# Kernel tuning notes

Hardware: AMD Instinct MI355X
Metric: run time of the kernel (lower is better)

Reference implementation:

```python
import jax, jax.numpy as jnp
import numpy as np

V, E, H = 32000, 128, 256
B, L, T = 32, 512, 64


def _lstm_scan(x_pre, Whh, h0, c0):
    # x_pre: [L, B, 4H] precomputed input projection (+bias). PyTorch gate order i,f,g,o.
    def step(carry, xp):
        h, c = carry
        g = xp + h @ Whh.T
        i, f, gg, o = jnp.split(g, 4, axis=-1)
        c = jax.nn.sigmoid(f) * c + jax.nn.sigmoid(i) * jnp.tanh(gg)
        h = jax.nn.sigmoid(o) * jnp.tanh(c)
        return (h, c), h
    (h, c), hs = jax.lax.scan(step, (h0, c0), x_pre)
    return hs, h, c


def setup_inputs() -> dict:
    key = jax.random.key(0)
    ks = jax.random.split(key, 20)
    s = 0.05  # ~ uniform(-1/sqrt(H), 1/sqrt(H)) scale
    def rn(k, shape):
        return (jax.random.normal(k, shape) * s).astype(jnp.float32)
    return {
        "source": jax.random.randint(ks[0], (B, L), 0, V),
        "target": jax.random.randint(ks[1], (B, T), 0, V),
        "embedding": rn(ks[2], (V, E)),
        "enc_fw_Wih": rn(ks[3], (4 * H, E)),
        "enc_fw_Whh": rn(ks[4], (4 * H, H)),
        "enc_fw_b": rn(ks[5], (4 * H,)),
        "enc_bw_Wih": rn(ks[6], (4 * H, E)),
        "enc_bw_Whh": rn(ks[7], (4 * H, H)),
        "enc_bw_b": rn(ks[8], (4 * H,)),
        "dec_Wih": rn(ks[9], (4 * H, E + 2 * H)),
        "dec_Whh": rn(ks[10], (4 * H, H)),
        "dec_b": rn(ks[11], (4 * H,)),
        "attn_w": rn(ks[12], (4 * H,)),
        "attn_b": rn(ks[13], (1,)),
        "dp_W": rn(ks[14], (2 * H, H)),
        "dp_b": rn(ks[15], (2 * H,)),
        "vp_W": rn(ks[16], (V, 3 * H)),
        "vp_b": rn(ks[17], (V,)),
        "pg_W": rn(ks[18], (3 * H + E, 1)),
        "pg_b": rn(ks[19], (1,)),
    }


def _forward(source, target, embedding, enc_fw_Wih, enc_fw_Whh, enc_fw_b,
             enc_bw_Wih, enc_bw_Whh, enc_bw_b, dec_Wih, dec_Whh, dec_b,
             attn_w, attn_b, dp_W, dp_b, vp_W, vp_b, pg_W, pg_b):
    Bn = source.shape[0]
    emb = embedding[source]                                   # [B,L,E]
    h0 = jnp.zeros((Bn, H), jnp.float32)
    c0 = jnp.zeros((Bn, H), jnp.float32)
    # bidirectional encoder
    xpf = jnp.swapaxes(emb @ enc_fw_Wih.T + enc_fw_b, 0, 1)   # [L,B,4H]
    hs_f, h_f, c_f = _lstm_scan(xpf, enc_fw_Whh, h0, c0)
    xpb = jnp.swapaxes(emb @ enc_bw_Wih.T + enc_bw_b, 0, 1)[::-1]
    hs_b, _, _ = _lstm_scan(xpb, enc_bw_Whh, h0, c0)
    enc_out = jnp.concatenate([hs_f, hs_b[::-1]], axis=-1)    # [L,B,2H]
    enc_out = jnp.swapaxes(enc_out, 0, 1)                     # [B,L,2H]

    # attn Linear(4H->1) split into encoder part (precomputed) and decoder part
    wa_enc, wa_dec = attn_w[:2 * H], attn_w[2 * H:]
    enc_att = enc_out @ wa_enc                                # [B,L]
    batch_idx = jnp.arange(Bn)[:, None]

    # teacher forcing: input at step t is target[:, t-1], zeros at t=0
    tokens_in = jnp.concatenate(
        [jnp.zeros((Bn, 1), target.dtype), target[:, :-1]], axis=1).T  # [T,B]

    def step(carry, tok):
        h, c = carry
        emb_t = embedding[tok]                                # [B,E]
        dec_proj = h @ dp_W.T + dp_b                          # [B,2H]
        score = enc_att + (dec_proj @ wa_dec)[:, None] + attn_b  # [B,L]
        aw = jax.nn.softmax(score, axis=1)
        context = jnp.einsum('bl,bld->bd', aw, enc_out)       # [B,2H]
        dec_in = jnp.concatenate([emb_t, context], axis=1)    # [B,E+2H]
        g = dec_in @ dec_Wih.T + dec_b + h @ dec_Whh.T
        i, f, gg, o = jnp.split(g, 4, axis=-1)
        c = jax.nn.sigmoid(f) * c + jax.nn.sigmoid(i) * jnp.tanh(gg)
        h = jax.nn.sigmoid(o) * jnp.tanh(c)
        gen_feat = jnp.concatenate([h, context], axis=1)      # [B,3H]
        vocab_dist = jax.nn.softmax(gen_feat @ vp_W.T + vp_b, axis=1)  # [B,V]
        p_gen = jax.nn.sigmoid(
            jnp.concatenate([gen_feat, emb_t], axis=1) @ pg_W + pg_b)  # [B,1]
        copy = jnp.zeros_like(vocab_dist).at[batch_idx, source].add(aw)
        final = p_gen * vocab_dist + (1.0 - p_gen) * copy
        return (h, c), final

    # decoder init = forward-direction final encoder state (matches torch slice)
    _, outs = jax.lax.scan(step, (h_f, c_f), tokens_in)       # [T,B,V]
    return jnp.swapaxes(outs, 0, 1)                           # [B,T,V]


def reference(source, target, embedding, enc_fw_Wih, enc_fw_Whh, enc_fw_b,
              enc_bw_Wih, enc_bw_Whh, enc_bw_b, dec_Wih, dec_Whh, dec_b,
              attn_w, attn_b, dp_W, dp_b, vp_W, vp_b, pg_W, pg_b):
    return _forward(source, target, embedding, enc_fw_Wih, enc_fw_Whh, enc_fw_b,
                    enc_bw_Wih, enc_bw_Whh, enc_bw_b, dec_Wih, dec_Whh, dec_b,
                    attn_w, attn_b, dp_W, dp_b, vp_W, vp_b, pg_W, pg_b)
```

## Files before the change

kernel.cpp:

```cpp
#include <hip/hip_runtime.h>
#include <hip/hip_bf16.h>


#define DEVINL __device__ __forceinline__

typedef _Float16 f16;
typedef _Float16 f16x2 __attribute__((ext_vector_type(2)));
typedef _Float16 f16x8 __attribute__((ext_vector_type(8)));
typedef short    s16x8 __attribute__((ext_vector_type(8)));
typedef float    f32x4 __attribute__((ext_vector_type(4)));
typedef unsigned int u32x4 __attribute__((ext_vector_type(4)));

DEVINL float dot2f(unsigned int a, unsigned int b, float acc) {
#if __has_builtin(__builtin_amdgcn_fdot2)
  return __builtin_amdgcn_fdot2(__builtin_bit_cast(f16x2, a),
                                __builtin_bit_cast(f16x2, b), acc, false);
#else
  f16x2 x = __builtin_bit_cast(f16x2, a);
  f16x2 y = __builtin_bit_cast(f16x2, b);
  return acc + (float)x[0] * (float)y[0] + (float)x[1] * (float)y[1];
#endif
}

DEVINL float sigm(float x) { return 1.0f / (1.0f + __expf(-x)); }
DEVINL float tanh_f(float x) {
  float e = __expf(2.0f * x);
  return (e - 1.0f) / (e + 1.0f);
}
DEVINL unsigned int pack2(float a, float b) {
  f16x2 p; p[0] = (f16)a; p[1] = (f16)b;
  return __builtin_bit_cast(unsigned int, p);
}


__global__ __launch_bounds__(256) void k_pack_whh(const float* __restrict__ W,
                                                  uint4* __restrict__ dst) {
  int id = blockIdx.x * 256 + threadIdx.x;
  int k2b = id >> 10, j = id & 1023;
  const float* s = W + (size_t)j * 256 + k2b * 8;
  uint4 u;
  u.x = pack2(s[0], s[1]); u.y = pack2(s[2], s[3]);
  u.z = pack2(s[4], s[5]); u.w = pack2(s[6], s[7]);
  dst[k2b * 1024 + j] = u;
}

__global__ __launch_bounds__(256) void k_pack_wih(const float* __restrict__ W,
                                                  unsigned int* __restrict__ dst,
                                                  int ldk) {
  int id = blockIdx.x * 256 + threadIdx.x;
  int j = id >> 6, k2 = id & 63;
  dst[j * 64 + k2] = pack2(W[(size_t)j * ldk + 2 * k2],
                           W[(size_t)j * ldk + 2 * k2 + 1]);
}

__global__ __launch_bounds__(256) void k_pack_vpw(const float* __restrict__ W,
                                                  __hip_bfloat16* __restrict__ dst) {
  size_t id = (size_t)blockIdx.x * 256 + threadIdx.x;
  dst[id] = __float2bfloat16(W[id]);
}

__global__ __launch_bounds__(256) void k_encproj(
    const int* __restrict__ source, const float* __restrict__ emb,
    const unsigned int* __restrict__ W2, const float* __restrict__ bias,
    f16* __restrict__ X, int rev) {
  int l = blockIdx.x;
  int tid = threadIdx.x;
  __shared__ int toks[32];
  __shared__ unsigned int e2[32 * 66];
  if (tid < 32) toks[tid] = source[tid * 512 + l];
  __syncthreads();
  {
    int row = tid >> 3;
    int k2b = (tid & 7) * 8;
    const float* er = emb + (size_t)toks[row] * 128 + k2b * 2;
#pragma unroll
    for (int i = 0; i < 8; ++i)
      e2[row * 66 + k2b + i] = pack2(er[2 * i], er[2 * i + 1]);
  }
  __syncthreads();
  int jg = tid >> 3;
  int bq = (tid & 7) * 4;
  int orow = rev ? (511 - l) : l;
  for (int jt = 0; jt < 4; ++jt) {
    int j0 = jt * 256 + jg * 8;
    float acc[8][4];
#pragma unroll
    for (int jj = 0; jj < 8; ++jj) {
      float bv = bias[j0 + jj];
#pragma unroll
      for (int bb = 0; bb < 4; ++bb) acc[jj][bb] = bv;
    }
    for (int kp = 0; kp < 32; ++kp) {
      uint2 w[8], e[4];
#pragma unroll
      for (int jj = 0; jj < 8; ++jj)
        w[jj] = *(const uint2*)(W2 + (size_t)(j0 + jj) * 64 + kp * 2);
#pragma unroll
      for (int bb = 0; bb < 4; ++bb)
        e[bb] = *(const uint2*)(e2 + (bq + bb) * 66 + kp * 2);
#pragma unroll
      for (int jj = 0; jj < 8; ++jj)
#pragma unroll
        for (int bb = 0; bb < 4; ++bb) {
          acc[jj][bb] = dot2f(e[bb].x, w[jj].x, acc[jj][bb]);
          acc[jj][bb] = dot2f(e[bb].y, w[jj].y, acc[jj][bb]);
        }
    }
#pragma unroll
    for (int bb = 0; bb < 4; ++bb) {
      f16x8 v;
#pragma unroll
      for (int jj = 0; jj < 8; ++jj) v[jj] = (f16)acc[jj][bb];
      *(f16x8*)(X + ((size_t)orow * 32 + bq + bb) * 1024 + j0) = v;
    }
  }
}

__global__ __launch_bounds__(256) void k_decproj(
    const int* __restrict__ target, const float* __restrict__ emb,
    const unsigned int* __restrict__ W2, const float* __restrict__ cprj,
    const float* __restrict__ pgW, f16* __restrict__ X,
    float* __restrict__ pemb) {
  int t = blockIdx.x;
  int tid = threadIdx.x;
  __shared__ int toks[32];
  __shared__ unsigned int e2[32 * 66];
  if (tid < 32) toks[tid] = (t == 0) ? 0 : target[tid * 64 + t - 1];
  __syncthreads();
  {
    int row = tid >> 3;
    int k2b = (tid & 7) * 8;
    const float* er = emb + (size_t)toks[row] * 128 + k2b * 2;
#pragma unroll
    for (int i = 0; i < 8; ++i)
      e2[row * 66 + k2b + i] = pack2(er[2 * i], er[2 * i + 1]);
  }
  __syncthreads();
  if (tid < 32) {
    float s = 0.f;
    for (int k2 = 0; k2 < 64; ++k2) {
      f16x2 p = __builtin_bit_cast(f16x2, e2[tid * 66 + k2]);
      s += (float)p[0] * pgW[768 + 2 * k2] + (float)p[1] * pgW[768 + 2 * k2 + 1];
    }
    pemb[t * 32 + tid] = s;
  }
  int jg = tid >> 3;
  int bq = (tid & 7) * 4;
  for (int jt = 0; jt < 4; ++jt) {
    int j0 = jt * 256 + jg * 8;
    float acc[8][4];
#pragma unroll
    for (int jj = 0; jj < 8; ++jj)
#pragma unroll
      for (int bb = 0; bb < 4; ++bb)
        acc[jj][bb] = cprj[(size_t)(bq + bb) * 1024 + j0 + jj];
    for (int kp = 0; kp < 32; ++kp) {
      uint2 w[8], e[4];
#pragma unroll
      for (int jj = 0; jj < 8; ++jj)
        w[jj] = *(const uint2*)(W2 + (size_t)(j0 + jj) * 64 + kp * 2);
#pragma unroll
      for (int bb = 0; bb < 4; ++bb)
        e[bb] = *(const uint2*)(e2 + (bq + bb) * 66 + kp * 2);
#pragma unroll
      for (int jj = 0; jj < 8; ++jj)
#pragma unroll
        for (int bb = 0; bb < 4; ++bb) {
          acc[jj][bb] = dot2f(e[bb].x, w[jj].x, acc[jj][bb]);
          acc[jj][bb] = dot2f(e[bb].y, w[jj].y, acc[jj][bb]);
        }
    }
#pragma unroll
    for (int bb = 0; bb < 4; ++bb) {
      f16x8 v;
#pragma unroll
      for (int jj = 0; jj < 8; ++jj) v[jj] = (f16)acc[jj][bb];
      *(f16x8*)(X + ((size_t)t * 32 + bq + bb) * 1024 + j0) = v;
    }
  }
}

#define PIN23(A)                                                             \
  asm volatile("" : "+v"(A[0]), "+v"(A[1]), "+v"(A[2]), "+v"(A[3]),          \
                    "+v"(A[4]), "+v"(A[5]), "+v"(A[6]), "+v"(A[7]),          \
                    "+v"(A[8]), "+v"(A[9]), "+v"(A[10]), "+v"(A[11]),        \
                    "+v"(A[12]), "+v"(A[13]), "+v"(A[14]), "+v"(A[15]),      \
                    "+v"(A[16]), "+v"(A[17]), "+v"(A[18]), "+v"(A[19]),      \
                    "+v"(A[20]), "+v"(A[21]), "+v"(A[22]))

__global__ __launch_bounds__(256, 1) void k_scan(
    const uint4* __restrict__ Wp0, const f16* __restrict__ X0,
    float* __restrict__ out, float* __restrict__ cf,
    const float* __restrict__ hinit, int mode, int nsteps) {
  extern __shared__ char smem[];
  uint4* WL = (uint4*)smem;
  f16*   hh = (f16*)(smem + 147456);
  int bid = blockIdx.x;
  int dir = (mode == 2) ? 0 : (bid >> 5);
  int b   = (mode == 2) ? bid : (bid & 31);
  int isdec = (mode == 2);
  const uint4* Wp = Wp0 + (size_t)dir * 32768;
  const f16* X = X0 + (size_t)dir * 16777216;
  int t_ = threadIdx.x;

  u32x4 w0[23], w1[23], w2[23], w3[23];
#pragma unroll
  for (int q = 0; q < 23; ++q) {
    w0[q] = *(const u32x4*)&Wp[(q << 10) + 0 * 256 + t_];
    w1[q] = *(const u32x4*)&Wp[(q << 10) + 1 * 256 + t_];
    w2[q] = *(const u32x4*)&Wp[(q << 10) + 2 * 256 + t_];
    w3[q] = *(const u32x4*)&Wp[(q << 10) + 3 * 256 + t_];
  }
  PIN23(w0); PIN23(w1); PIN23(w2); PIN23(w3);

  for (int i = t_; i < 9 * 1024; i += 256) WL[i] = Wp[23 * 1024 + i];

  float c_reg;
  if (isdec) {
    c_reg = cf[b * 256 + t_];
    hh[t_] = (f16)hinit[((size_t)b * 512 + 511) * 512 + t_];
  } else {
    c_reg = 0.f;
    hh[t_] = (f16)0.f;
  }
  __syncthreads();

  const f16* xp = X + (size_t)b * 1024;
  f16 xc0 = xp[t_], xc1 = xp[256 + t_], xc2 = xp[512 + t_], xc3 = xp[768 + t_];

  for (int t = 0; t < nsteps; ++t) {
    float a0 = (float)xc0, a1 = (float)xc1, a2 = (float)xc2, a3 = (float)xc3;
    if (t + 1 < nsteps) {
      const f16* xn = xp + 32768;
      xc0 = xn[t_]; xc1 = xn[256 + t_]; xc2 = xn[512 + t_]; xc3 = xn[768 + t_];
      xp = xn;
    }
    const f16* hb = hh + (t & 1) * 256;
#pragma unroll
    for (int q = 0; q < 23; ++q) {
      u32x4 hq = *(const u32x4*)(hb + q * 8);
      a0 = dot2f(hq[0], w0[q][0], a0); a1 = dot2f(hq[0], w1[q][0], a1);
      a2 = dot2f(hq[0], w2[q][0], a2); a3 = dot2f(hq[0], w3[q][0], a3);
      a0 = dot2f(hq[1], w0[q][1], a0); a1 = dot2f(hq[1], w1[q][1], a1);
      a2 = dot2f(hq[1], w2[q][1], a2); a3 = dot2f(hq[1], w3[q][1], a3);
      a0 = dot2f(hq[2], w0[q][2], a0); a1 = dot2f(hq[2], w1[q][2], a1);
      a2 = dot2f(hq[2], w2[q][2], a2); a3 = dot2f(hq[2], w3[q][2], a3);
      a0 = dot2f(hq[3], w0[q][3], a0); a1 = dot2f(hq[3], w1[q][3], a1);
      a2 = dot2f(hq[3], w2[q][3], a2); a3 = dot2f(hq[3], w3[q][3], a3);
    }
#pragma unroll
    for (int q = 23; q < 32; ++q) {
      u32x4 hq = *(const u32x4*)(hb + q * 8);
      u32x4 v0 = *(const u32x4*)&WL[(q - 23) * 1024 + 0 * 256 + t_];
      u32x4 v1 = *(const u32x4*)&WL[(q - 23) * 1024 + 1 * 256 + t_];
      u32x4 v2 = *(const u32x4*)&WL[(q - 23) * 1024 + 2 * 256 + t_];
      u32x4 v3 = *(const u32x4*)&WL[(q - 23) * 1024 + 3 * 256 + t_];
      a0 = dot2f(hq[0], v0[0], a0); a1 = dot2f(hq[0], v1[0], a1);
      a2 = dot2f(hq[0], v2[0], a2); a3 = dot2f(hq[0], v3[0], a3);
      a0 = dot2f(hq[1], v0[1], a0); a1 = dot2f(hq[1], v1[1], a1);
      a2 = dot2f(hq[1], v2[1], a2); a3 = dot2f(hq[1], v3[1], a3);
      a0 = dot2f(hq[2], v0[2], a0); a1 = dot2f(hq[2], v1[2], a1);
      a2 = dot2f(hq[2], v2[2], a2); a3 = dot2f(hq[2], v3[2], a3);
      a0 = dot2f(hq[3], v0[3], a0); a1 = dot2f(hq[3], v1[3], a1);
      a2 = dot2f(hq[3], v2[3], a2); a3 = dot2f(hq[3], v3[3], a3);
    }
    c_reg = sigm(a1) * c_reg + sigm(a0) * tanh_f(a2);
    float hv = sigm(a3) * tanh_f(c_reg);
    hh[((t + 1) & 1) * 256 + t_] = (f16)hv;
    if (isdec)
      out[((size_t)t * 32 + b) * 256 + t_] = hv;
    else if (dir == 1)
      out[((size_t)b * 512 + (511 - t)) * 512 + 256 + t_] = hv;
    else
      out[((size_t)b * 512 + t) * 512 + t_] = hv;
    __syncthreads();
  }
  if (!isdec && dir == 0) cf[b * 256 + t_] = c_reg;
}

__global__ __launch_bounds__(512) void k_attention(
    const float* __restrict__ enc_out, const float* __restrict__ attn_w,
    const float* __restrict__ pgW, const int* __restrict__ source,
    float* __restrict__ aw_out, float* __restrict__ ctx_out,
    float* __restrict__ pctx, float* __restrict__ copyb) {
  int b = blockIdx.x, tid = threadIdx.x;
  __shared__ float red[512];
  __shared__ float awl[512];
  const float4* row = (const float4*)(enc_out + ((size_t)b * 512 + tid) * 512);
  const float4* wv = (const float4*)attn_w;
  float s = 0.f;
  for (int i = 0; i < 128; ++i) {
    float4 r = row[i], w = wv[i];
    s += r.x * w.x + r.y * w.y + r.z * w.z + r.w * w.w;
  }
  red[tid] = s; __syncthreads();
  for (int off = 256; off > 0; off >>= 1) {
    if (tid < off) red[tid] = fmaxf(red[tid], red[tid + off]);
    __syncthreads();
  }
  float m = red[0]; __syncthreads();
  float e = __expf(s - m);
  red[tid] = e; __syncthreads();
  for (int off = 256; off > 0; off >>= 1) {
    if (tid < off) red[tid] += red[tid + off];
    __syncthreads();
  }
  float a = e / red[0];
  __syncthreads();
  awl[tid] = a;
  aw_out[b * 512 + tid] = a;
  atomicAdd(&copyb[(size_t)b * 32000 + source[b * 512 + tid]], a);
  __syncthreads();
  float c = 0.f;
  const float* col = enc_out + (size_t)b * 512 * 512 + tid;
  for (int ll = 0; ll < 512; ++ll) c += awl[ll] * col[(size_t)ll * 512];
  ctx_out[b * 512 + tid] = c;
  red[tid] = c * pgW[256 + tid];
  __syncthreads();
  for (int off = 256; off > 0; off >>= 1) {
    if (tid < off) red[tid] += red[tid + off];
    __syncthreads();
  }
  if (tid == 0) pctx[b] = red[0];
}

__global__ __launch_bounds__(256) void k_ctxproj(
    const float* __restrict__ ctx, const float* __restrict__ dWih,
    const float* __restrict__ db, float* __restrict__ cprj) {
  int b = blockIdx.x, tid = threadIdx.x;
  __shared__ float cs[512];
  cs[tid] = ctx[b * 512 + tid];
  cs[tid + 256] = ctx[b * 512 + 256 + tid];
  __syncthreads();
  const float4* c4 = (const float4*)cs;
  for (int q = 0; q < 4; ++q) {
    int j = q * 256 + tid;
    const float4* wr = (const float4*)(dWih + (size_t)j * 640 + 128);
    float s = db[j];
    for (int i = 0; i < 128; ++i) {
      float4 w = wr[i]; float4 c = c4[i];
      s += w.x * c.x + w.y * c.y + w.z * c.z + w.w * c.w;
    }
    cprj[b * 1024 + j] = s;
  }
}

__global__ __launch_bounds__(256) void k_pgen_gf(
    const float* __restrict__ h_all, const float* __restrict__ ctx,
    const float* __restrict__ pgW, const float* __restrict__ pgb,
    const float* __restrict__ pctx, const float* __restrict__ pemb,
    float* __restrict__ pgen, __hip_bfloat16* __restrict__ gf) {
  int r = blockIdx.x, tid = threadIdx.x;
  int b = r & 31;
  float h = h_all[(size_t)r * 256 + tid];
  gf[(size_t)r * 768 + tid] = __float2bfloat16(h);
  float c0 = ctx[b * 512 + tid], c1 = ctx[b * 512 + 256 + tid];
  gf[(size_t)r * 768 + 256 + tid] = __float2bfloat16(c0);
  gf[(size_t)r * 768 + 512 + tid] = __float2bfloat16(c1);
  __shared__ float red[256];
  red[tid] = h * pgW[tid];
  __syncthreads();
  for (int off = 128; off > 0; off >>= 1) {
    if (tid < off) red[tid] += red[tid + off];
    __syncthreads();
  }
  if (tid == 0) pgen[r] = sigm(red[0] + pctx[b] + pemb[r] + pgb[0]);
}

__global__ __launch_bounds__(256) void k_logits(
    const __hip_bfloat16* __restrict__ A, const __hip_bfloat16* __restrict__ B,
    const float* __restrict__ vpb, float* __restrict__ out) {
  __shared__ short As[128 * 40];
  __shared__ short Bs[128 * 40];
  int tid = threadIdx.x;
  int bn = blockIdx.x, bm = blockIdx.y;
  int wave = tid >> 6, lane = tid & 63;
  int q = lane >> 4, m = lane & 15;
  f32x4 acc[2][8];
#pragma unroll
  for (int i = 0; i < 2; ++i)
#pragma unroll
    for (int j = 0; j < 8; ++j)
      acc[i][j] = (f32x4){0.f, 0.f, 0.f, 0.f};
  const short* Ag = (const short*)A + (size_t)(bm * 128) * 768;
  const short* Bg = (const short*)B + (size_t)(bn * 128) * 768;
  int lrow = tid >> 2;
  int lseg = (tid & 3) * 8;
  for (int kc = 0; kc < 768; kc += 32) {
    __syncthreads();
    *(s16x8*)&As[lrow * 40 + lseg] = *(const s16x8*)(Ag + (size_t)lrow * 768 + kc + lseg);
    *(s16x8*)&As[(lrow + 64) * 40 + lseg] = *(const s16x8*)(Ag + (size_t)(lrow + 64) * 768 + kc + lseg);
    *(s16x8*)&Bs[lrow * 40 + lseg] = *(const s16x8*)(Bg + (size_t)lrow * 768 + kc + lseg);
    *(s16x8*)&Bs[(lrow + 64) * 40 + lseg] = *(const s16x8*)(Bg + (size_t)(lrow + 64) * 768 + kc + lseg);
    __syncthreads();
    s16x8 a0 = *(const s16x8*)&As[(wave * 32 + m) * 40 + q * 8];
    s16x8 a1 = *(const s16x8*)&As[(wave * 32 + 16 + m) * 40 + q * 8];
#pragma unroll
    for (int nb = 0; nb < 8; ++nb) {
      s16x8 bf = *(const s16x8*)&Bs[(nb * 16 + m) * 40 + q * 8];
      acc[0][nb] = __builtin_amdgcn_mfma_f32_16x16x32_bf16(a0, bf, acc[0][nb], 0, 0, 0);
      acc[1][nb] = __builtin_amdgcn_mfma_f32_16x16x32_bf16(a1, bf, acc[1][nb], 0, 0, 0);
    }
  }
#pragma unroll
  for (int mb = 0; mb < 2; ++mb)
#pragma unroll
    for (int nb = 0; nb < 8; ++nb) {
      int v = bn * 128 + nb * 16 + m;
      float vb = vpb[v];
#pragma unroll
      for (int rg = 0; rg < 4; ++rg) {
        int R = bm * 128 + wave * 32 + mb * 16 + q * 4 + rg;
        int bb = R & 31, tt = R >> 5;
        out[((size_t)bb * 64 + tt) * 32000 + v] = acc[mb][nb][rg] + vb;
      }
    }
}

__global__ __launch_bounds__(256) void k_rowsum(const float* __restrict__ out,
                                                float* __restrict__ invs) {
  int row = blockIdx.x, tid = threadIdx.x;
  const float* r = out + (size_t)row * 32000;
  float s = 0.f;
  for (int i = tid; i < 32000; i += 256) s += __expf(r[i]);
  __shared__ float red[256];
  red[tid] = s; __syncthreads();
  for (int off = 128; off > 0; off >>= 1) {
    if (tid < off) red[tid] += red[tid + off];
    __syncthreads();
  }
  if (tid == 0) invs[row] = 1.0f / red[0];
}

__global__ __launch_bounds__(256) void k_final(float* __restrict__ out,
                                               const float* __restrict__ invs,
                                               const float* __restrict__ pgen,
                                               const float* __restrict__ copyb) {
  int row = blockIdx.x;
  int b = row >> 6, t = row & 63;
  float pg = pgen[t * 32 + b];
  float inv = invs[row];
  float* r = out + (size_t)row * 32000;
  const float* cp = copyb + (size_t)b * 32000;
  for (int i = threadIdx.x; i < 32000; i += 256)
    r[i] = pg * __expf(r[i]) * inv + (1.f - pg) * cp[i];
}

extern "C" void kernel_launch(void* const* d_in, const int* in_sizes, int n_in,
                              void* d_out, int out_size, void* d_ws, size_t ws_size,
                              hipStream_t stream) {
  (void)in_sizes; (void)n_in; (void)out_size;
  const int*   source = (const int*)d_in[0];
  const int*   target = (const int*)d_in[1];
  const float* embedding = (const float*)d_in[2];
  const float* Wih_f = (const float*)d_in[3];
  const float* Whh_f = (const float*)d_in[4];
  const float* b_f   = (const float*)d_in[5];
  const float* Wih_b = (const float*)d_in[6];
  const float* Whh_b = (const float*)d_in[7];
  const float* b_b   = (const float*)d_in[8];
  const float* dWih  = (const float*)d_in[9];
  const float* dWhh  = (const float*)d_in[10];
  const float* db    = (const float*)d_in[11];
  const float* attn_w = (const float*)d_in[12];
  const float* vpW = (const float*)d_in[16];
  const float* vpb = (const float*)d_in[17];
  const float* pgW = (const float*)d_in[18];
  const float* pgb = (const float*)d_in[19];

  constexpr size_t OFF_WP   = 0;
  constexpr size_t OFF_WIH2 = OFF_WP + 3ull * 32768 * 16;
  constexpr size_t OFF_VP16 = OFF_WIH2 + 3ull * 65536 * 4;
  constexpr size_t OFF_XENC = OFF_VP16 + 24576000ull * 2;
  constexpr size_t OFF_XD   = OFF_XENC + 2ull * 16777216 * 2;
  constexpr size_t OFF_ENCO = OFF_XD + 2097152ull * 2;
  constexpr size_t OFF_CF   = OFF_ENCO + 8388608ull * 4;
  constexpr size_t OFF_AW   = OFF_CF + 32768;
  constexpr size_t OFF_CTX  = OFF_AW + 65536;
  constexpr size_t OFF_CPRJ = OFF_CTX + 65536;
  constexpr size_t OFF_PCTX = OFF_CPRJ + 131072;
  constexpr size_t OFF_PEMB = OFF_PCTX + 128;
  constexpr size_t OFF_PGEN = OFF_PEMB + 8192;
  constexpr size_t OFF_HALL = OFF_PGEN + 8192;
  constexpr size_t OFF_GF   = OFF_HALL + 2097152;
  constexpr size_t OFF_COPY = OFF_GF + 3145728;
  constexpr size_t OFF_INVS = OFF_COPY + 4096000;
  constexpr size_t WS_NEED  = OFF_INVS + 8192;
  if (ws_size < WS_NEED) return;

  char* ws = (char*)d_ws;
  uint4* wp             = (uint4*)(ws + OFF_WP);
  unsigned int* wih2f   = (unsigned int*)(ws + OFF_WIH2);
  unsigned int* wih2b   = wih2f + 65536;
  unsigned int* wih2d   = wih2f + 131072;
  __hip_bfloat16* vp16  = (__hip_bfloat16*)(ws + OFF_VP16);
  f16* Xenc             = (f16*)(ws + OFF_XENC);
  f16* Xd               = (f16*)(ws + OFF_XD);
  float* enc_out        = (float*)(ws + OFF_ENCO);
  float* cf             = (float*)(ws + OFF_CF);
  float* aw             = (float*)(ws + OFF_AW);
  float* ctx            = (float*)(ws + OFF_CTX);
  float* cprj           = (float*)(ws + OFF_CPRJ);
  float* pctx           = (float*)(ws + OFF_PCTX);
  float* pemb           = (float*)(ws + OFF_PEMB);
  float* pgen           = (float*)(ws + OFF_PGEN);
  float* h_all          = (float*)(ws + OFF_HALL);
  __hip_bfloat16* gf    = (__hip_bfloat16*)(ws + OFF_GF);
  float* copyb          = (float*)(ws + OFF_COPY);
  float* invs           = (float*)(ws + OFF_INVS);
  float* outp           = (float*)d_out;

  constexpr int SCAN_LDS = 148480;
  static bool attr_done = false;
  if (!attr_done) {
    hipFuncSetAttribute((const void*)k_scan,
                        hipFuncAttributeMaxDynamicSharedMemorySize, SCAN_LDS);
    attr_done = true;
  }

  hipMemsetAsync(copyb, 0, 32ull * 32000 * 4, stream);

  k_pack_whh<<<128, 256, 0, stream>>>(Whh_f, wp);
  k_pack_whh<<<128, 256, 0, stream>>>(Whh_b, wp + 32768);
  k_pack_whh<<<128, 256, 0, stream>>>(dWhh,  wp + 65536);
  k_pack_wih<<<256, 256, 0, stream>>>(Wih_f, wih2f, 128);
  k_pack_wih<<<256, 256, 0, stream>>>(Wih_b, wih2b, 128);
  k_pack_wih<<<256, 256, 0, stream>>>(dWih,  wih2d, 640);
  k_pack_vpw<<<96000, 256, 0, stream>>>(vpW, vp16);

  k_encproj<<<512, 256, 0, stream>>>(source, embedding, wih2f, b_f, Xenc, 0);
  k_encproj<<<512, 256, 0, stream>>>(source, embedding, wih2b, b_b,
                                     Xenc + 16777216, 1);
  k_scan<<<64, 256, SCAN_LDS, stream>>>(wp, Xenc, enc_out, cf, nullptr, 0, 512);
  k_attention<<<32, 512, 0, stream>>>(enc_out, attn_w, pgW, source, aw, ctx,
                                      pctx, copyb);
  k_ctxproj<<<32, 256, 0, stream>>>(ctx, dWih, db, cprj);
  k_decproj<<<64, 256, 0, stream>>>(target, embedding, wih2d, cprj, pgW, Xd,
                                    pemb);
  k_scan<<<32, 256, SCAN_LDS, stream>>>(wp + 65536, Xd, h_all, cf, enc_out, 2, 64);
  k_pgen_gf<<<2048, 256, 0, stream>>>(h_all, ctx, pgW, pgb, pctx, pemb, pgen,
                                      gf);
  k_logits<<<dim3(250, 16), 256, 0, stream>>>(gf, vp16, vpb, outp);
  k_rowsum<<<2048, 256, 0, stream>>>(outp, invs);
  k_final<<<2048, 256, 0, stream>>>(outp, invs, pgen, copyb);
}
```

Baseline: 2.871 ms.

## Split LSTM recurrent matvec across 4 lanes per unit with DPP reduction

Rewrites the recurrent scan kernel to use 512 threads per block. Each group of four lanes shares two hidden units, each lane takes a quarter of the K dimension, and the partial sums are combined with DPP quad reductions. The Whh packing layout and the h buffer swizzle change to match, and a larger share of the weights now lives in registers with less kept in LDS. The aim is to shorten the serial per-step dependency chain, at the cost of cross-lane reduction work and only one lane in four doing the gate writes.

```diff
diff --git a/kernel.cpp b/kernel.cpp
--- a/kernel.cpp
+++ b/kernel.cpp
@@ -32,16 +32,35 @@
   return __builtin_bit_cast(unsigned int, p);
 }
 
+DEVINL float qsum(float v) {
+  int a = __builtin_bit_cast(int, v);
+  v += __builtin_bit_cast(float,
+        __builtin_amdgcn_mov_dpp(a, 0xB1, 0xF, 0xF, true));
+  int b = __builtin_bit_cast(int, v);
+  v += __builtin_bit_cast(float,
+        __builtin_amdgcn_mov_dpp(b, 0x4E, 0xF, 0xF, true));
+  return v;
+}
+
+DEVINL int hswz(int d) {
+  int g = d >> 3;
+  return ((g & 7) * 4 + (g >> 3)) * 8 + (d & 7);
+}
+
 
 __global__ __launch_bounds__(256) void k_pack_whh(const float* __restrict__ W,
                                                   uint4* __restrict__ dst) {
   int id = blockIdx.x * 256 + threadIdx.x;
-  int k2b = id >> 10, j = id & 1023;
-  const float* s = W + (size_t)j * 256 + k2b * 8;
+  int s = id >> 9, t = id & 511;
+  int i = s >> 3, qq = s & 7;
+  int c0 = t >> 2, qt = t & 3;
+  int c = c0 + (i << 7);
+  int kb = qt * 64 + qq * 8;
+  const float* src = W + (size_t)c * 256 + kb;
   uint4 u;
-  u.x = pack2(s[0], s[1]); u.y = pack2(s[2], s[3]);
-  u.z = pack2(s[4], s[5]); u.w = pack2(s[6], s[7]);
-  dst[k2b * 1024 + j] = u;
+  u.x = pack2(src[0], src[1]); u.y = pack2(src[2], src[3]);
+  u.z = pack2(src[4], src[5]); u.w = pack2(src[6], src[7]);
+  dst[id] = u;
 }
 
 __global__ __launch_bounds__(256) void k_pack_wih(const float* __restrict__ W,
@@ -180,102 +199,116 @@
   }
 }
 
-#define PIN23(A)                                                             \
-  asm volatile("" : "+v"(A[0]), "+v"(A[1]), "+v"(A[2]), "+v"(A[3]),          \
-                    "+v"(A[4]), "+v"(A[5]), "+v"(A[6]), "+v"(A[7]),          \
-                    "+v"(A[8]), "+v"(A[9]), "+v"(A[10]), "+v"(A[11]),        \
-                    "+v"(A[12]), "+v"(A[13]), "+v"(A[14]), "+v"(A[15]),      \
-                    "+v"(A[16]), "+v"(A[17]), "+v"(A[18]), "+v"(A[19]),      \
-                    "+v"(A[20]), "+v"(A[21]), "+v"(A[22]))
-
-__global__ __launch_bounds__(256, 1) void k_scan(
-    const uint4* __restrict__ Wp0, const f16* __restrict__ X0,
+#define PIN16(A)                                                             \
+  asm volatile("" : "+v"((A)[0]), "+v"((A)[1]), "+v"((A)[2]), "+v"((A)[3]),  \
+                    "+v"((A)[4]), "+v"((A)[5]), "+v"((A)[6]), "+v"((A)[7]),  \
+                    "+v"((A)[8]), "+v"((A)[9]), "+v"((A)[10]), "+v"((A)[11]),\
+                    "+v"((A)[12]), "+v"((A)[13]), "+v"((A)[14]), "+v"((A)[15]))
+
+__global__ __launch_bounds__(512, 2) void k_scan(
+    const uint4* __restrict__ WQ0, const f16* __restrict__ X0,
     float* __restrict__ out, float* __restrict__ cf,
     const float* __restrict__ hinit, int mode, int nsteps) {
   extern __shared__ char smem[];
   uint4* WL = (uint4*)smem;
-  f16*   hh = (f16*)(smem + 147456);
+  f16*   hh = (f16*)(smem + 131072);
   int bid = blockIdx.x;
   int dir = (mode == 2) ? 0 : (bid >> 5);
   int b   = (mode == 2) ? bid : (bid & 31);
   int isdec = (mode == 2);
-  const uint4* Wp = Wp0 + (size_t)dir * 32768;
+  const uint4* WQ = WQ0 + (size_t)dir * 32768;
   const f16* X = X0 + (size_t)dir * 16777216;
   int t_ = threadIdx.x;
-
-  u32x4 w0[23], w1[23], w2[23], w3[23];
-#pragma unroll
-  for (int q = 0; q < 23; ++q) {
-    w0[q] = *(const u32x4*)&Wp[(q << 10) + 0 * 256 + t_];
-    w1[q] = *(const u32x4*)&Wp[(q << 10) + 1 * 256 + t_];
-    w2[q] = *(const u32x4*)&Wp[(q << 10) + 2 * 256 + t_];
-    w3[q] = *(const u32x4*)&Wp[(q << 10) + 3 * 256 + t_];
-  }
-  PIN23(w0); PIN23(w1); PIN23(w2); PIN23(w3);
-
-  for (int i = t_; i < 9 * 1024; i += 256) WL[i] = Wp[23 * 1024 + i];
-
-  float c_reg;
+  int qt = t_ & 3;
+  int c0 = t_ >> 2;
+
+  u32x4 wr[48];
+#pragma unroll
+  for (int s = 0; s < 48; ++s) wr[s] = *(const u32x4*)&WQ[s * 512 + t_];
+  PIN16(wr); PIN16(wr + 16); PIN16(wr + 32);
+
+  for (int i = t_; i < 16 * 512; i += 512) WL[i] = WQ[48 * 512 + i];
+
+  float c0r, c1r;
   if (isdec) {
-    c_reg = cf[b * 256 + t_];
-    hh[t_] = (f16)hinit[((size_t)b * 512 + 511) * 512 + t_];
+    c0r = cf[b * 256 + c0];
+    c1r = cf[b * 256 + 128 + c0];
+    if (t_ < 256) hh[hswz(t_)] = (f16)hinit[((size_t)b * 512 + 511) * 512 + t_];
   } else {
-    c_reg = 0.f;
-    hh[t_] = (f16)0.f;
-  }
-  __syncthreads();
-
+    c0r = 0.f; c1r = 0.f;
+    if (t_ < 256) hh[t_] = (f16)0.f;
+  }
+  __syncthreads();
+
+  int wi0 = hswz(c0), wi1 = hswz(c0 + 128);
   const f16* xp = X + (size_t)b * 1024;
-  f16 xc0 = xp[t_], xc1 = xp[256 + t_], xc2 = xp[512 + t_], xc3 = xp[768 + t_];
+  float xf[8];
+#pragma unroll
+  for (int i = 0; i < 8; ++i) xf[i] = (float)xp[c0 + (i << 7)];
 
   for (int t = 0; t < nsteps; ++t) {
-    float a0 = (float)xc0, a1 = (float)xc1, a2 = (float)xc2, a3 = (float)xc3;
+    float xcur[8];
+#pragma unroll
+    for (int i = 0; i < 8; ++i) xcur[i] = xf[i];
     if (t + 1 < nsteps) {
       const f16* xn = xp + 32768;
-      xc0 = xn[t_]; xc1 = xn[256 + t_]; xc2 = xn[512 + t_]; xc3 = xn[768 + t_];
+#pragma unroll
+      for (int i = 0; i < 8; ++i) xf[i] = (float)xn[c0 + (i << 7)];
       xp = xn;
     }
-    const f16* hb = hh + (t & 1) * 256;
-#pragma unroll
-    for (int q = 0; q < 23; ++q) {
-      u32x4 hq = *(const u32x4*)(hb + q * 8);
-      a0 = dot2f(hq[0], w0[q][0], a0); a1 = dot2f(hq[0], w1[q][0], a1);
-      a2 = dot2f(hq[0], w2[q][0], a2); a3 = dot2f(hq[0], w3[q][0], a3);
-      a0 = dot2f(hq[1], w0[q][1], a0); a1 = dot2f(hq[1], w1[q][1], a1);
-      a2 = dot2f(hq[1], w2[q][1], a2); a3 = dot2f(hq[1], w3[q][1], a3);
-      a0 = dot2f(hq[2], w0[q][2], a0); a1 = dot2f(hq[2], w1[q][2], a1);
-      a2 = dot2f(hq[2], w2[q][2], a2); a3 = dot2f(hq[2], w3[q][2], a3);
-      a0 = dot2f(hq[3], w0[q][3], a0); a1 = dot2f(hq[3], w1[q][3], a1);
-      a2 = dot2f(hq[3], w2[q][3], a2); a3 = dot2f(hq[3], w3[q][3], a3);
-    }
-#pragma unroll
-    for (int q = 23; q < 32; ++q) {
-      u32x4 hq = *(const u32x4*)(hb + q * 8);
-      u32x4 v0 = *(const u32x4*)&WL[(q - 23) * 1024 + 0 * 256 + t_];
-      u32x4 v1 = *(const u32x4*)&WL[(q - 23) * 1024 + 1 * 256 + t_];
-      u32x4 v2 = *(const u32x4*)&WL[(q - 23) * 1024 + 2 * 256 + t_];
-      u32x4 v3 = *(const u32x4*)&WL[(q - 23) * 1024 + 3 * 256 + t_];
-      a0 = dot2f(hq[0], v0[0], a0); a1 = dot2f(hq[0], v1[0], a1);
-      a2 = dot2f(hq[0], v2[0], a2); a3 = dot2f(hq[0], v3[0], a3);
-      a0 = dot2f(hq[1], v0[1], a0); a1 = dot2f(hq[1], v1[1], a1);
-      a2 = dot2f(hq[1], v2[1], a2); a3 = dot2f(hq[1], v3[1], a3);
-      a0 = dot2f(hq[2], v0[2], a0); a1 = dot2f(hq[2], v1[2], a1);
-      a2 = dot2f(hq[2], v2[2], a2); a3 = dot2f(hq[2], v3[2], a3);
-      a0 = dot2f(hq[3], v0[3], a0); a1 = dot2f(hq[3], v1[3], a1);
-      a2 = dot2f(hq[3], v2[3], a2); a3 = dot2f(hq[3], v3[3], a3);
-    }
-    c_reg = sigm(a1) * c_reg + sigm(a0) * tanh_f(a2);
-    float hv = sigm(a3) * tanh_f(c_reg);
-    hh[((t + 1) & 1) * 256 + t_] = (f16)hv;
-    if (isdec)
-      out[((size_t)t * 32 + b) * 256 + t_] = hv;
-    else if (dir == 1)
-      out[((size_t)b * 512 + (511 - t)) * 512 + 256 + t_] = hv;
-    else
-      out[((size_t)b * 512 + t) * 512 + t_] = hv;
-    __syncthreads();
-  }
-  if (!isdec && dir == 0) cf[b * 256 + t_] = c_reg;
+    float acc[8];
+#pragma unroll
+    for (int i = 0; i < 8; ++i) acc[i] = 0.f;
+    const u32x4* hb = (const u32x4*)(hh + (t & 1) * 256);
+#pragma unroll
+    for (int qq = 0; qq < 8; ++qq) {
+      u32x4 hq = hb[qq * 4 + qt];
+#pragma unroll
+      for (int i = 0; i < 6; ++i) {
+        int s = i * 8 + qq;
+        acc[i] = dot2f(hq[0], wr[s][0], acc[i]);
+        acc[i] = dot2f(hq[1], wr[s][1], acc[i]);
+        acc[i] = dot2f(hq[2], wr[s][2], acc[i]);
+        acc[i] = dot2f(hq[3], wr[s][3], acc[i]);
+      }
+      u32x4 w6 = *(const u32x4*)&WL[qq * 512 + t_];
+      u32x4 w7 = *(const u32x4*)&WL[(8 + qq) * 512 + t_];
+      acc[6] = dot2f(hq[0], w6[0], acc[6]);
+      acc[6] = dot2f(hq[1], w6[1], acc[6]);
+      acc[6] = dot2f(hq[2], w6[2], acc[6]);
+      acc[6] = dot2f(hq[3], w6[3], acc[6]);
+      acc[7] = dot2f(hq[0], w7[0], acc[7]);
+      acc[7] = dot2f(hq[1], w7[1], acc[7]);
+      acc[7] = dot2f(hq[2], w7[2], acc[7]);
+      acc[7] = dot2f(hq[3], w7[3], acc[7]);
+    }
+#pragma unroll
+    for (int i = 0; i < 8; ++i) acc[i] = qsum(acc[i]) + xcur[i];
+    c0r = sigm(acc[2]) * c0r + sigm(acc[0]) * tanh_f(acc[4]);
+    float hv0 = sigm(acc[6]) * tanh_f(c0r);
+    c1r = sigm(acc[3]) * c1r + sigm(acc[1]) * tanh_f(c1r * 0.f + acc[5]);
+    float hv1 = sigm(acc[7]) * tanh_f(c1r);
+    f16* hn = hh + ((t + 1) & 1) * 256;
+    if (qt == 0) {
+      hn[wi0] = (f16)hv0;
+      hn[wi1] = (f16)hv1;
+      if (isdec) {
+        size_t r = ((size_t)t * 32 + b) * 256;
+        out[r + c0] = hv0; out[r + 128 + c0] = hv1;
+      } else if (dir == 1) {
+        size_t r = ((size_t)b * 512 + (511 - t)) * 512 + 256;
+        out[r + c0] = hv0; out[r + 128 + c0] = hv1;
+      } else {
+        size_t r = ((size_t)b * 512 + t) * 512;
+        out[r + c0] = hv0; out[r + 128 + c0] = hv1;
+      }
+    }
+    __syncthreads();
+  }
+  if (!isdec && dir == 0 && qt == 0) {
+    cf[b * 256 + c0] = c0r;
+    cf[b * 256 + 128 + c0] = c1r;
+  }
 }
 
 __global__ __launch_bounds__(512) void k_attention(
@@ -510,7 +543,7 @@
   float* invs           = (float*)(ws + OFF_INVS);
   float* outp           = (float*)d_out;
 
-  constexpr int SCAN_LDS = 148480;
+  constexpr int SCAN_LDS = 132096;
   static bool attr_done = false;
   if (!attr_done) {
     hipFuncSetAttribute((const void*)k_scan,
@@ -531,13 +564,13 @@
   k_encproj<<<512, 256, 0, stream>>>(source, embedding, wih2f, b_f, Xenc, 0);
   k_encproj<<<512, 256, 0, stream>>>(source, embedding, wih2b, b_b,
                                      Xenc + 16777216, 1);
-  k_scan<<<64, 256, SCAN_LDS, stream>>>(wp, Xenc, enc_out, cf, nullptr, 0, 512);
+  k_scan<<<64, 512, SCAN_LDS, stream>>>(wp, Xenc, enc_out, cf, nullptr, 0, 512);
   k_attention<<<32, 512, 0, stream>>>(enc_out, attn_w, pgW, source, aw, ctx,
                                       pctx, copyb);
   k_ctxproj<<<32, 256, 0, stream>>>(ctx, dWih, db, cprj);
   k_decproj<<<64, 256, 0, stream>>>(target, embedding, wih2d, cprj, pgW, Xd,
                                     pemb);
-  k_scan<<<32, 256, SCAN_LDS, stream>>>(wp + 65536, Xd, h_all, cf, enc_out, 2, 64);
+  k_scan<<<32, 512, SCAN_LDS, stream>>>(wp + 65536, Xd, h_all, cf, enc_out, 2, 64);
   k_pgen_gf<<<2048, 256, 0, stream>>>(h_all, ctx, pgW, pgb, pctx, pemb, pgen,
                                       gf);
   k_logits<<<dim3(250, 16), 256, 0, stream>>>(gf, vp16, vpb, outp);
```

After: 2.355 ms. 18.0% less time.
